# Performance work log

Measured on AMD Instinct MI355X. Metric: run time of the kernel, lower is better.

The kernel has to match this reference:

```python
import jax, jax.numpy as jnp
import numpy as np

NUM_HEADS = 16
NUM_KV_HEADS = 4
HEAD_DIM = 64
HIDDEN = 1024
B, S = 2, 2048


def setup_inputs() -> dict:
    key = jax.random.key(0)
    ks = jax.random.split(key, 9)
    sc = 0.02
    return {
        "x": jax.random.normal(ks[0], (B, S, HIDDEN), dtype=jnp.float32),
        "Wq": jax.random.normal(ks[1], (HIDDEN, NUM_HEADS * HEAD_DIM), dtype=jnp.float32) * sc,
        "bq": jnp.zeros((NUM_HEADS * HEAD_DIM,), dtype=jnp.float32),
        "Wk": jax.random.normal(ks[2], (HIDDEN, NUM_KV_HEADS * HEAD_DIM), dtype=jnp.float32) * sc,
        "bk": jnp.zeros((NUM_KV_HEADS * HEAD_DIM,), dtype=jnp.float32),
        "Wv": jax.random.normal(ks[3], (HIDDEN, NUM_KV_HEADS * HEAD_DIM), dtype=jnp.float32) * sc,
        "bv": jnp.zeros((NUM_KV_HEADS * HEAD_DIM,), dtype=jnp.float32),
        "Wo": jax.random.normal(ks[4], (NUM_HEADS * HEAD_DIM, HIDDEN), dtype=jnp.float32) * sc,
        "bo": jnp.zeros((HIDDEN,), dtype=jnp.float32),
    }


def reference(x, Wq, bq, Wk, bk, Wv, bv, Wo, bo):
    bs, seq, _ = x.shape
    groups = NUM_HEADS // NUM_KV_HEADS
    # projections -> [B, H, S, D]
    q = (x @ Wq + bq).reshape(bs, seq, NUM_HEADS, HEAD_DIM).transpose(0, 2, 1, 3)
    k = (x @ Wk + bk).reshape(bs, seq, NUM_KV_HEADS, HEAD_DIM).transpose(0, 2, 1, 3)
    v = (x @ Wv + bv).reshape(bs, seq, NUM_KV_HEADS, HEAD_DIM).transpose(0, 2, 1, 3)
    # repeat_interleave KV heads to match query heads (GQA expansion)
    k = jnp.repeat(k, groups, axis=1)
    v = jnp.repeat(v, groups, axis=1)
    # NOTE: source applies NO 1/sqrt(d) scaling and no mask/ALiBi
    scores = jnp.einsum("bhqd,bhkd->bhqk", q, k)
    attn = jax.nn.softmax(scores.astype(jnp.float32), axis=-1).astype(q.dtype)
    out = jnp.einsum("bhqk,bhkd->bhqd", attn, v)
    out = out.transpose(0, 2, 1, 3).reshape(bs, seq, NUM_HEADS * HEAD_DIM)
    return out @ Wo + bo
```

## Files before the change

kernel.cpp:

```cpp
#include <hip/hip_runtime.h>

#define NHEADS 16
#define NKV    4
#define HDIM   64
#define HIDDEN 1024
#define BATCH  2
#define SEQ    2048
#define MROWS  (BATCH * SEQ)
#define LOG2E  1.44269504088896340736f

typedef __bf16 bf16_t;
typedef bf16_t bf16x8 __attribute__((ext_vector_type(8)));
typedef float  f32x4  __attribute__((ext_vector_type(4)));

template<int N>  struct ic { static constexpr int  v = N; };
template<bool B> struct bc { static constexpr bool v = B; };

__device__ __forceinline__ float bf2f(unsigned short u) {
    return __uint_as_float(((unsigned int)u) << 16);
}
__device__ __forceinline__ unsigned short f2bf(float f) {
    unsigned int u = __float_as_uint(f);
    u += 0x7FFFu + ((u >> 16) & 1u);
    return (unsigned short)(u >> 16);
}

__device__ __forceinline__ void gld16(const unsigned short* g, unsigned short* l)
{
    __builtin_amdgcn_global_load_lds(
        (const __attribute__((address_space(1))) void*)g,
        (__attribute__((address_space(3))) void*)l,
        16, 0, 0);
}

__device__ __forceinline__ int swz(int row, int ch) {
    return (row * 8 + (ch ^ (row & 7))) * 8;
}

__device__ __forceinline__ bool sniff_is_f32(const unsigned short* __restrict__ x)
{
    const int e = (x[threadIdx.x & 63] >> 7) & 0xFF;
    const unsigned long long ok = __ballot(e >= 110 && e <= 140);
    return __popcll(ok) < 56;
}

__device__ __forceinline__ void load8cvt(const void* base, size_t elem, bool isf32, unsigned short out[8])
{
    if (!isf32) {
        *(uint4*)out = *(const uint4*)((const unsigned short*)base + elem);
    } else {
        const float* p = (const float*)base + elem;
        float4 v0 = *(const float4*)p;
        float4 v1 = *(const float4*)(p + 4);
        out[0] = f2bf(v0.x); out[1] = f2bf(v0.y); out[2] = f2bf(v0.z); out[3] = f2bf(v0.w);
        out[4] = f2bf(v1.x); out[5] = f2bf(v1.y); out[6] = f2bf(v1.z); out[7] = f2bf(v1.w);
    }
}
__device__ __forceinline__ float bias_at(const void* b, int i, bool isf32)
{
    return isf32 ? ((const float*)b)[i] : bf2f(((const unsigned short*)b)[i]);
}

__global__ __launch_bounds__(256)
void prep_kernel(const void* __restrict__ x,
                 const void* __restrict__ Wq, const void* __restrict__ Wk,
                 const void* __restrict__ Wv, const void* __restrict__ Wo,
                 unsigned short* __restrict__ xb,
                 unsigned short* __restrict__ Wqkvt,
                 unsigned short* __restrict__ Wot)
{
    const bool isf32 = sniff_is_f32((const unsigned short*)x);
    const int t = threadIdx.x;
    int bid = blockIdx.x;

    if (bid < 2048) {
        if (!isf32) return;
        const size_t c = (size_t)bid * 256 + t;
        unsigned short v[8];
        load8cvt(x, c * 8, true, v);
        *(uint4*)(&xb[c * 8]) = *(uint4*)v;
        return;
    }
    bid -= 2048;
    const void* src; unsigned short* dst; int N, rowoff;
    if (bid < 256)      {             src = Wq; dst = Wqkvt; N = 1024; rowoff = 0;    }
    else if (bid < 320) { bid -= 256; src = Wk; dst = Wqkvt; N = 256;  rowoff = 1024; }
    else if (bid < 384) { bid -= 320; src = Wv; dst = Wqkvt; N = 256;  rowoff = 1280; }
    else                { bid -= 384; src = Wo; dst = Wot;   N = 1024; rowoff = 0;    }
    const int ntx = N / 64;
    const int gn0 = (bid % ntx) * 64;
    const int gk0 = (bid / ntx) * 64;

    __shared__ unsigned short Ts[64][72];
#pragma unroll
    for (int half = 0; half < 2; ++half) {
        const int kl = (t >> 3) + half * 32;
        const int n8 = (t & 7) * 8;
        unsigned short v[8];
        load8cvt(src, (size_t)(gk0 + kl) * N + gn0 + n8, isf32, v);
        *(uint4*)(&Ts[kl][n8]) = *(uint4*)v;
    }
    __syncthreads();
#pragma unroll
    for (int half = 0; half < 2; ++half) {
        const int nl = (t >> 3) + half * 32;
        const int k8 = (t & 7) * 8;
        unsigned short v[8];
#pragma unroll
        for (int j = 0; j < 8; ++j) v[j] = Ts[k8 + j][nl];
        *(uint4*)(&dst[(size_t)(rowoff + gn0 + nl) * HIDDEN + gk0 + k8]) = *(uint4*)v;
    }
}

template<int AI, int BJ, int KK>
__device__ __forceinline__ void gemm_tile(const unsigned short* __restrict__ A,
                                          const unsigned short* __restrict__ Bt,
                                          int m0, int n0,
                                          unsigned short* As, unsigned short* Bs,
                                          f32x4 (&acc)[AI][BJ])
{
    const int tid  = threadIdx.x;
    const int lane = tid & 63;
    const int wave = tid >> 6;
    const int quad = lane >> 4;
    const int l15  = lane & 15;
    const int wr   = wave >> 1;
    const int wc   = wave & 1;

    const int srow = tid >> 3;
    const int gch  = ((tid & 7) ^ (srow & 7)) * 8;

    const unsigned short* ga[AI];
    const unsigned short* gb[BJ];
#pragma unroll
    for (int r = 0; r < AI; ++r) ga[r] = A  + (size_t)(m0 + r * 32 + srow) * KK + gch;
#pragma unroll
    for (int r = 0; r < BJ; ++r) gb[r] = Bt + (size_t)(n0 + r * 32 + srow) * KK + gch;

    unsigned short* const adst = As + wave * 512;
    unsigned short* const bdst = Bs + wave * 512;

    int aoffs[2][AI], boffs[2][BJ];
#pragma unroll
    for (int kk = 0; kk < 2; ++kk) {
#pragma unroll
        for (int i = 0; i < AI; ++i) aoffs[kk][i] = swz(wr * (AI * 16) + i * 16 + l15, kk * 4 + quad);
#pragma unroll
        for (int j = 0; j < BJ; ++j) boffs[kk][j] = swz(wc * (BJ * 16) + j * 16 + l15, kk * 4 + quad);
    }

    auto stage = [&](int buf) {
#pragma unroll
        for (int r = 0; r < AI; ++r) { gld16(ga[r], adst + buf * (AI * 2048) + r * 2048); ga[r] += 64; }
#pragma unroll
        for (int r = 0; r < BJ; ++r) { gld16(gb[r], bdst + buf * (BJ * 2048) + r * 2048); gb[r] += 64; }
    };

    constexpr int nk = KK / 64;
    stage(0);
#pragma unroll 2
    for (int k = 0; k < nk; ++k) {
        const int cur = k & 1;
        __syncthreads();
        if (k + 1 < nk) stage(cur ^ 1);

#pragma unroll
        for (int kk = 0; kk < 2; ++kk) {
            bf16x8 af[AI], bfv[BJ];
#pragma unroll
            for (int i = 0; i < AI; ++i) af[i]  = *(const bf16x8*)(&As[cur * (AI * 2048) + aoffs[kk][i]]);
#pragma unroll
            for (int j = 0; j < BJ; ++j) bfv[j] = *(const bf16x8*)(&Bs[cur * (BJ * 2048) + boffs[kk][j]]);
            __builtin_amdgcn_s_setprio(1);
#pragma unroll
            for (int i = 0; i < AI; ++i)
#pragma unroll
                for (int j = 0; j < BJ; ++j)
                    acc[i][j] = __builtin_amdgcn_mfma_f32_16x16x32_bf16(af[i], bfv[j], acc[i][j], 0, 0, 0);
            __builtin_amdgcn_s_setprio(0);
        }
    }
}

__global__ __launch_bounds__(256)
void gemm_qkv(const void* __restrict__ xraw,
              const unsigned short* __restrict__ xb,
              const unsigned short* __restrict__ Bt,
              const void* __restrict__ bq, const void* __restrict__ bk,
              const void* __restrict__ bv,
              unsigned short* __restrict__ Qh,
              unsigned short* __restrict__ Kh,
              unsigned short* __restrict__ Vt)
{
    __shared__ __align__(16) unsigned short As[2 * 128 * 64];
    __shared__ __align__(16) unsigned short Bs[2 * 96 * 64];
    const bool bias_f32 = sniff_is_f32((const unsigned short*)xraw);
    const unsigned short* A = bias_f32 ? xb : (const unsigned short*)xraw;
    const int lane = threadIdx.x & 63;
    const int wave = threadIdx.x >> 6;
    const int quad = lane >> 4, l15 = lane & 15;
    const int wr = wave >> 1, wc = wave & 1;
    const int m0 = blockIdx.y * 128, n0 = blockIdx.x * 96;

    f32x4 acc[4][3] = {};
    gemm_tile<4, 3, HIDDEN>(A, Bt, m0, n0, As, Bs, acc);

#pragma unroll
    for (int i = 0; i < 4; ++i) {
#pragma unroll
        for (int j = 0; j < 3; ++j) {
            const int nn  = n0 + wc * 48 + j * 16 + l15;
            const int mmb = m0 + wr * 64 + i * 16 + quad * 4;
            const int b = mmb >> 11, s0 = mmb & 2047;
            if (nn < 1024) {
                const float bias = bias_at(bq, nn, bias_f32);
                const int h = nn >> 6, d = nn & 63;
                const size_t idx0 = (((size_t)(b * NHEADS + h)) * SEQ + s0) * 64 + d;
#pragma unroll
                for (int r = 0; r < 4; ++r)
                    Qh[idx0 + (size_t)r * 64] = f2bf((acc[i][j][r] + bias) * LOG2E);
            } else if (nn < 1280) {
                const int nk = nn - 1024;
                const float bias = bias_at(bk, nk, bias_f32);
                const int h = nk >> 6, d = nk & 63;
                const size_t idx0 = (((size_t)(b * NKV + h)) * SEQ + s0) * 64 + d;
#pragma unroll
                for (int r = 0; r < 4; ++r)
                    Kh[idx0 + (size_t)r * 64] = f2bf(acc[i][j][r] + bias);
            } else {
                const int nv = nn - 1280;
                const float bias = bias_at(bv, nv, bias_f32);
                const int h = nv >> 6, d = nv & 63;
                const size_t idx = (((size_t)(b * NKV + h)) * 64 + d) * SEQ + s0;
                unsigned short vv[4];
#pragma unroll
                for (int r = 0; r < 4; ++r) vv[r] = f2bf(acc[i][j][r] + bias);
                *(uint2*)(&Vt[idx]) = *(uint2*)vv;
            }
        }
    }
}

__global__ __launch_bounds__(256)
void gemm_o(const void* __restrict__ xraw,
            const unsigned short* __restrict__ A,
            const unsigned short* __restrict__ Bt,
            const void* __restrict__ bo,
            float* __restrict__ out)
{
    __shared__ __align__(16) unsigned short As[2 * 128 * 64];
    __shared__ __align__(16) unsigned short Bs[2 * 64 * 64];
    const bool bias_f32 = sniff_is_f32((const unsigned short*)xraw);
    const int lane = threadIdx.x & 63;
    const int wave = threadIdx.x >> 6;
    const int quad = lane >> 4, l15 = lane & 15;
    const int wr = wave >> 1, wc = wave & 1;
    const int m0 = blockIdx.y * 128, n0 = blockIdx.x * 64;

    f32x4 acc[4][2] = {};
    gemm_tile<4, 2, HIDDEN>(A, Bt, m0, n0, As, Bs, acc);

#pragma unroll
    for (int i = 0; i < 4; ++i) {
#pragma unroll
        for (int j = 0; j < 2; ++j) {
            const int nn = n0 + wc * 32 + j * 16 + l15;
            const float bvv = bias_at(bo, nn, bias_f32);
#pragma unroll
            for (int r = 0; r < 4; ++r) {
                const int mm = m0 + wr * 64 + i * 16 + quad * 4 + r;
                out[(size_t)mm * HIDDEN + nn] = acc[i][j][r] + bvv;
            }
        }
    }
}

#define NT    (SEQ / 64)
#define KVOFF (64 * 64)

__global__ __launch_bounds__(256)
void attn_kernel(const unsigned short* __restrict__ Qh,
                 const unsigned short* __restrict__ Kh,
                 const unsigned short* __restrict__ Vt,
                 unsigned short* __restrict__ O)
{
    __shared__ __align__(16) unsigned short Kth[3 * KVOFF];
    __shared__ __align__(16) unsigned short VtT[3 * KVOFF];
    __shared__ __align__(16) unsigned short Pt[4 * 32 * 64];

    const int tid  = threadIdx.x;
    const int lane = tid & 63;
    const int wave = tid >> 6;
    const int quad = lane >> 4;
    const int l15  = lane & 15;

    const int qt = blockIdx.x;
    const int h  = blockIdx.y;
    const int b  = blockIdx.z;
    const int kv = h >> 2;

    const size_t qoff = ((size_t)(b * NHEADS + h)) * SEQ * HDIM;
    const size_t koff = ((size_t)(b * NKV + kv)) * SEQ * HDIM;
    const size_t voff = ((size_t)(b * NKV + kv)) * HDIM * SEQ;

    const int q0 = qt * 128 + wave * 32;

    bf16x8 qf0[2], qf1[2];
#pragma unroll
    for (int qs = 0; qs < 2; ++qs) {
        const size_t qrow = qoff + (size_t)(q0 + qs * 16 + l15) * HDIM;
        qf0[qs] = *(const bf16x8*)(&Qh[qrow + quad * 8]);
        qf1[qs] = *(const bf16x8*)(&Qh[qrow + 32 + quad * 8]);
    }

    bf16x8 onesv;
#pragma unroll
    for (int i = 0; i < 8; ++i) onesv[i] = (bf16_t)1.0f;

    f32x4 o0[4] = {}, o1[4] = {};
    f32x4 lacc0 = {}, lacc1 = {};

    int koff0[4], koff1[4], pwoff[2][4], proff[2], voffs[2][4];
#pragma unroll
    for (int j = 0; j < 4; ++j) {
        koff0[j] = swz(j * 16 + l15, quad);
        koff1[j] = swz(j * 16 + l15, quad ^ 4);
#pragma unroll
        for (int qs = 0; qs < 2; ++qs)
            pwoff[qs][j] = wave * 2048 + swz(qs * 16 + l15, j * 2 + (quad >> 1)) + (quad & 1) * 4;
    }
#pragma unroll
    for (int kk = 0; kk < 2; ++kk) {
        proff[kk] = wave * 2048 + swz(l15, kk * 4 + quad);
#pragma unroll
        for (int dt = 0; dt < 4; ++dt)
            voffs[kk][dt] = swz(dt * 16 + l15, kk * 4 + quad);
    }

    const unsigned short* kp = Kh + koff;
    const unsigned short* vp = Vt + voff;
    const int srow0 = tid >> 3;
    const int gch_s = ((tid & 7) ^ (srow0 & 7)) * 8;
    unsigned short* const kdst = Kth + wave * 512;
    unsigned short* const vdst = VtT + wave * 512;

#define ATTN_STAGE(B)                                                               \
    do {                                                                            \
        gld16(kp + (size_t)srow0 * HDIM + gch_s,        kdst + (B) * KVOFF);        \
        gld16(kp + (size_t)(srow0 + 32) * HDIM + gch_s, kdst + (B) * KVOFF + 2048); \
        gld16(vp + (size_t)srow0 * SEQ + gch_s,         vdst + (B) * KVOFF);        \
        gld16(vp + (size_t)(srow0 + 32) * SEQ + gch_s,  vdst + (B) * KVOFF + 2048); \
        kp += 64 * HDIM; vp += 64;                                                  \
    } while (0)

    ATTN_STAGE(0);
    ATTN_STAGE(1);

    auto step = [&](auto B_, auto STG_, auto LAST_) {
        constexpr int B = decltype(B_)::v;
        if constexpr (decltype(LAST_)::v) asm volatile("s_waitcnt vmcnt(0)" ::: "memory");
        else                              asm volatile("s_waitcnt vmcnt(4)" ::: "memory");
        __builtin_amdgcn_sched_barrier(0);
        __builtin_amdgcn_s_barrier();
        __builtin_amdgcn_sched_barrier(0);
        if constexpr (decltype(STG_)::v) ATTN_STAGE((B + 2) % 3);

#pragma unroll
        for (int j = 0; j < 4; ++j) {
            const bf16x8 kh0 = *(const bf16x8*)(&Kth[B * KVOFF + koff0[j]]);
            const bf16x8 kh1 = *(const bf16x8*)(&Kth[B * KVOFF + koff1[j]]);
#pragma unroll
            for (int qs = 0; qs < 2; ++qs) {
                f32x4 z = {};
                __builtin_amdgcn_s_setprio(1);
                z = __builtin_amdgcn_mfma_f32_16x16x32_bf16(kh0, qs ? qf0[1] : qf0[0], z, 0, 0, 0);
                const f32x4 sc = __builtin_amdgcn_mfma_f32_16x16x32_bf16(kh1, qs ? qf1[1] : qf1[0], z, 0, 0, 0);
                __builtin_amdgcn_s_setprio(0);
                const float p0 = __builtin_amdgcn_exp2f(sc[0]);
                const float p1 = __builtin_amdgcn_exp2f(sc[1]);
                const float p2 = __builtin_amdgcn_exp2f(sc[2]);
                const float p3 = __builtin_amdgcn_exp2f(sc[3]);
                uint2 w;
                w.x = __builtin_amdgcn_perm(__float_as_uint(p1), __float_as_uint(p0), 0x07060302u);
                w.y = __builtin_amdgcn_perm(__float_as_uint(p3), __float_as_uint(p2), 0x07060302u);
                *(uint2*)(&Pt[pwoff[qs][j]]) = w;
            }
        }

#pragma unroll
        for (int kk = 0; kk < 2; ++kk) {
            const bf16x8 pf0 = *(const bf16x8*)(&Pt[proff[kk]]);
            const bf16x8 pf1 = *(const bf16x8*)(&Pt[proff[kk] + 1024]);
            __builtin_amdgcn_s_setprio(1);
            lacc0 = __builtin_amdgcn_mfma_f32_16x16x32_bf16(onesv, pf0, lacc0, 0, 0, 0);
            lacc1 = __builtin_amdgcn_mfma_f32_16x16x32_bf16(onesv, pf1, lacc1, 0, 0, 0);
#pragma unroll
            for (int dt = 0; dt < 4; ++dt) {
                const bf16x8 vf = *(const bf16x8*)(&VtT[B * KVOFF + voffs[kk][dt]]);
                o0[dt] = __builtin_amdgcn_mfma_f32_16x16x32_bf16(vf, pf0, o0[dt], 0, 0, 0);
                o1[dt] = __builtin_amdgcn_mfma_f32_16x16x32_bf16(vf, pf1, o1[dt], 0, 0, 0);
            }
            __builtin_amdgcn_s_setprio(0);
        }
    };

#pragma unroll 1
    for (int t0 = 0; t0 < 30; t0 += 3) {
        step(ic<0>{}, bc<true>{}, bc<false>{});
        step(ic<1>{}, bc<true>{}, bc<false>{});
        step(ic<2>{}, bc<true>{}, bc<false>{});
    }
    step(ic<0>{}, bc<false>{}, bc<false>{});
    step(ic<1>{}, bc<false>{}, bc<true>{});
#undef ATTN_STAGE

#pragma unroll
    for (int qs = 0; qs < 2; ++qs) {
        const float inv = 1.0f / (qs ? lacc1[0] : lacc0[0]);
        const size_t rowbase = ((size_t)b * SEQ + (q0 + qs * 16 + l15)) * (NHEADS * HDIM) + h * HDIM;
#pragma unroll
        for (int dt = 0; dt < 4; ++dt) {
            const f32x4 ov = qs ? o1[dt] : o0[dt];
            unsigned short v4[4];
#pragma unroll
            for (int r = 0; r < 4; ++r) v4[r] = f2bf(ov[r] * inv);
            *(uint2*)(&O[rowbase + dt * 16 + quad * 4]) = *(uint2*)v4;
        }
    }
}

extern "C" void kernel_launch(void* const* d_in, const int* in_sizes, int n_in,
                              void* d_out, int out_size, void* d_ws, size_t ws_size,
                              hipStream_t stream)
{
    const void* x  = d_in[0];
    const void* Wq = d_in[1];
    const void* bq = d_in[2];
    const void* Wk = d_in[3];
    const void* bk = d_in[4];
    const void* Wv = d_in[5];
    const void* bv = d_in[6];
    const void* Wo = d_in[7];
    const void* bo = d_in[8];
    float* out = (float*)d_out;

    unsigned short* p = (unsigned short*)d_ws;
    unsigned short* xb    = p; p += (size_t)MROWS * HIDDEN;
    unsigned short* Wqkvt = p; p += (size_t)1536 * HIDDEN;
    unsigned short* Wot   = p; p += (size_t)HIDDEN * HIDDEN;
    unsigned short* Qh = p;  p += (size_t)MROWS * 1024;
    unsigned short* Kh = p;  p += (size_t)2 * NKV * SEQ * HDIM;
    unsigned short* Vt = p;  p += (size_t)2 * NKV * SEQ * HDIM;
    unsigned short* A2 = p;  p += (size_t)MROWS * 1024;

    dim3 blk(256);
    prep_kernel<<<dim3(2688), blk, 0, stream>>>(x, Wq, Wk, Wv, Wo, xb, Wqkvt, Wot);
    gemm_qkv<<<dim3(1536 / 96, MROWS / 128), blk, 0, stream>>>(
        x, xb, Wqkvt, bq, bk, bv, Qh, Kh, Vt);
    attn_kernel<<<dim3(SEQ / 128, NHEADS, BATCH), blk, 0, stream>>>(Qh, Kh, Vt, A2);
    gemm_o<<<dim3(1024 / 64, MROWS / 128), blk, 0, stream>>>(x, A2, Wot, bo, out);
}
```

Before: 177.8 us.

## Load K fragments directly into registers in attention; shrink QKV GEMM N-tile

The attention kernel stops staging K tiles through LDS and instead loads each wave's K MFMA fragments straight from global memory into a double-buffered register set, while V keeps its three-stage LDS pipeline. The wait counts and the step schedule are rewritten to interleave the two buffer rotations. This drops LDS traffic and shared memory use for K, at the cost of redundant global reads of K by all four waves and more VGPRs. Separately, the QKV GEMM tile width goes from 96 to 64 columns, giving more blocks.

```diff
diff --git a/kernel.cpp b/kernel.cpp
--- a/kernel.cpp
+++ b/kernel.cpp
@@ -193,23 +193,23 @@
               unsigned short* __restrict__ Vt)
 {
     __shared__ __align__(16) unsigned short As[2 * 128 * 64];
-    __shared__ __align__(16) unsigned short Bs[2 * 96 * 64];
+    __shared__ __align__(16) unsigned short Bs[2 * 64 * 64];
     const bool bias_f32 = sniff_is_f32((const unsigned short*)xraw);
     const unsigned short* A = bias_f32 ? xb : (const unsigned short*)xraw;
     const int lane = threadIdx.x & 63;
     const int wave = threadIdx.x >> 6;
     const int quad = lane >> 4, l15 = lane & 15;
     const int wr = wave >> 1, wc = wave & 1;
-    const int m0 = blockIdx.y * 128, n0 = blockIdx.x * 96;
-
-    f32x4 acc[4][3] = {};
-    gemm_tile<4, 3, HIDDEN>(A, Bt, m0, n0, As, Bs, acc);
+    const int m0 = blockIdx.y * 128, n0 = blockIdx.x * 64;
+
+    f32x4 acc[4][2] = {};
+    gemm_tile<4, 2, HIDDEN>(A, Bt, m0, n0, As, Bs, acc);
 
 #pragma unroll
     for (int i = 0; i < 4; ++i) {
 #pragma unroll
-        for (int j = 0; j < 3; ++j) {
-            const int nn  = n0 + wc * 48 + j * 16 + l15;
+        for (int j = 0; j < 2; ++j) {
+            const int nn  = n0 + wc * 32 + j * 16 + l15;
             const int mmb = m0 + wr * 64 + i * 16 + quad * 4;
             const int b = mmb >> 11, s0 = mmb & 2047;
             if (nn < 1024) {
@@ -284,7 +284,6 @@
                  const unsigned short* __restrict__ Vt,
                  unsigned short* __restrict__ O)
 {
-    __shared__ __align__(16) unsigned short Kth[3 * KVOFF];
     __shared__ __align__(16) unsigned short VtT[3 * KVOFF];
     __shared__ __align__(16) unsigned short Pt[4 * 32 * 64];
 
@@ -320,15 +319,12 @@
     f32x4 o0[4] = {}, o1[4] = {};
     f32x4 lacc0 = {}, lacc1 = {};
 
-    int koff0[4], koff1[4], pwoff[2][4], proff[2], voffs[2][4];
-#pragma unroll
-    for (int j = 0; j < 4; ++j) {
-        koff0[j] = swz(j * 16 + l15, quad);
-        koff1[j] = swz(j * 16 + l15, quad ^ 4);
+    int pwoff[2][4], proff[2], voffs[2][4];
+#pragma unroll
+    for (int j = 0; j < 4; ++j)
 #pragma unroll
         for (int qs = 0; qs < 2; ++qs)
             pwoff[qs][j] = wave * 2048 + swz(qs * 16 + l15, j * 2 + (quad >> 1)) + (quad & 1) * 4;
-    }
 #pragma unroll
     for (int kk = 0; kk < 2; ++kk) {
         proff[kk] = wave * 2048 + swz(l15, kk * 4 + quad);
@@ -337,44 +333,55 @@
             voffs[kk][dt] = swz(dt * 16 + l15, kk * 4 + quad);
     }
 
-    const unsigned short* kp = Kh + koff;
-    const unsigned short* vp = Vt + voff;
+    const unsigned short* kfp = Kh + koff + (size_t)l15 * HDIM + quad * 8;
+    const unsigned short* vp  = Vt + voff;
     const int srow0 = tid >> 3;
     const int gch_s = ((tid & 7) ^ (srow0 & 7)) * 8;
-    unsigned short* const kdst = Kth + wave * 512;
     unsigned short* const vdst = VtT + wave * 512;
 
-#define ATTN_STAGE(B)                                                               \
-    do {                                                                            \
-        gld16(kp + (size_t)srow0 * HDIM + gch_s,        kdst + (B) * KVOFF);        \
-        gld16(kp + (size_t)(srow0 + 32) * HDIM + gch_s, kdst + (B) * KVOFF + 2048); \
-        gld16(vp + (size_t)srow0 * SEQ + gch_s,         vdst + (B) * KVOFF);        \
-        gld16(vp + (size_t)(srow0 + 32) * SEQ + gch_s,  vdst + (B) * KVOFF + 2048); \
-        kp += 64 * HDIM; vp += 64;                                                  \
+    bf16x8 kr0[2][4], kr1[2][4];
+
+#define KLOAD(KB)                                                                \
+    do {                                                                         \
+        _Pragma("unroll")                                                        \
+        for (int j = 0; j < 4; ++j) {                                            \
+            kr0[KB][j] = *(const bf16x8*)(kfp + j * (16 * HDIM));                \
+            kr1[KB][j] = *(const bf16x8*)(kfp + j * (16 * HDIM) + 32);           \
+        }                                                                        \
+        kfp += 64 * HDIM;                                                        \
     } while (0)
 
-    ATTN_STAGE(0);
-    ATTN_STAGE(1);
-
-    auto step = [&](auto B_, auto STG_, auto LAST_) {
-        constexpr int B = decltype(B_)::v;
+#define VSTAGE(B)                                                                \
+    do {                                                                         \
+        gld16(vp + (size_t)srow0 * SEQ + gch_s,        vdst + (B) * KVOFF);      \
+        gld16(vp + (size_t)(srow0 + 32) * SEQ + gch_s, vdst + (B) * KVOFF + 2048); \
+        vp += 64;                                                                \
+    } while (0)
+
+    VSTAGE(0);
+    KLOAD(0);
+    VSTAGE(1);
+
+    auto step = [&](auto VB_, auto KB_, auto SV_, auto SK_, auto LAST_) {
+        constexpr int VB = decltype(VB_)::v;
+        constexpr int KB = decltype(KB_)::v;
         if constexpr (decltype(LAST_)::v) asm volatile("s_waitcnt vmcnt(0)" ::: "memory");
-        else                              asm volatile("s_waitcnt vmcnt(4)" ::: "memory");
+        else                              asm volatile("s_waitcnt vmcnt(10)" ::: "memory");
         __builtin_amdgcn_sched_barrier(0);
         __builtin_amdgcn_s_barrier();
         __builtin_amdgcn_sched_barrier(0);
-        if constexpr (decltype(STG_)::v) ATTN_STAGE((B + 2) % 3);
+        if constexpr (decltype(SK_)::v) KLOAD(KB ^ 1);
+        if constexpr (decltype(SV_)::v) VSTAGE((VB + 2) % 3);
+        __builtin_amdgcn_sched_barrier(0);
 
 #pragma unroll
         for (int j = 0; j < 4; ++j) {
-            const bf16x8 kh0 = *(const bf16x8*)(&Kth[B * KVOFF + koff0[j]]);
-            const bf16x8 kh1 = *(const bf16x8*)(&Kth[B * KVOFF + koff1[j]]);
 #pragma unroll
             for (int qs = 0; qs < 2; ++qs) {
                 f32x4 z = {};
                 __builtin_amdgcn_s_setprio(1);
-                z = __builtin_amdgcn_mfma_f32_16x16x32_bf16(kh0, qs ? qf0[1] : qf0[0], z, 0, 0, 0);
-                const f32x4 sc = __builtin_amdgcn_mfma_f32_16x16x32_bf16(kh1, qs ? qf1[1] : qf1[0], z, 0, 0, 0);
+                z = __builtin_amdgcn_mfma_f32_16x16x32_bf16(kr0[KB][j], qs ? qf0[1] : qf0[0], z, 0, 0, 0);
+                const f32x4 sc = __builtin_amdgcn_mfma_f32_16x16x32_bf16(kr1[KB][j], qs ? qf1[1] : qf1[0], z, 0, 0, 0);
                 __builtin_amdgcn_s_setprio(0);
                 const float p0 = __builtin_amdgcn_exp2f(sc[0]);
                 const float p1 = __builtin_amdgcn_exp2f(sc[1]);
@@ -396,7 +403,7 @@
             lacc1 = __builtin_amdgcn_mfma_f32_16x16x32_bf16(onesv, pf1, lacc1, 0, 0, 0);
 #pragma unroll
             for (int dt = 0; dt < 4; ++dt) {
-                const bf16x8 vf = *(const bf16x8*)(&VtT[B * KVOFF + voffs[kk][dt]]);
+                const bf16x8 vf = *(const bf16x8*)(&VtT[VB * KVOFF + voffs[kk][dt]]);
                 o0[dt] = __builtin_amdgcn_mfma_f32_16x16x32_bf16(vf, pf0, o0[dt], 0, 0, 0);
                 o1[dt] = __builtin_amdgcn_mfma_f32_16x16x32_bf16(vf, pf1, o1[dt], 0, 0, 0);
             }
@@ -405,14 +412,18 @@
     };
 
 #pragma unroll 1
-    for (int t0 = 0; t0 < 30; t0 += 3) {
-        step(ic<0>{}, bc<true>{}, bc<false>{});
-        step(ic<1>{}, bc<true>{}, bc<false>{});
-        step(ic<2>{}, bc<true>{}, bc<false>{});
-    }
-    step(ic<0>{}, bc<false>{}, bc<false>{});
-    step(ic<1>{}, bc<false>{}, bc<true>{});
-#undef ATTN_STAGE
+    for (int t0 = 0; t0 < 30; t0 += 6) {
+        step(ic<0>{}, ic<0>{}, bc<true>{}, bc<true>{}, bc<false>{});
+        step(ic<1>{}, ic<1>{}, bc<true>{}, bc<true>{}, bc<false>{});
+        step(ic<2>{}, ic<0>{}, bc<true>{}, bc<true>{}, bc<false>{});
+        step(ic<0>{}, ic<1>{}, bc<true>{}, bc<true>{}, bc<false>{});
+        step(ic<1>{}, ic<0>{}, bc<true>{}, bc<true>{}, bc<false>{});
+        step(ic<2>{}, ic<1>{}, bc<true>{}, bc<true>{}, bc<false>{});
+    }
+    step(ic<0>{}, ic<0>{}, bc<false>{}, bc<true>{},  bc<false>{});
+    step(ic<1>{}, ic<1>{}, bc<false>{}, bc<false>{}, bc<true>{});
+#undef KLOAD
+#undef VSTAGE
 
 #pragma unroll
     for (int qs = 0; qs < 2; ++qs) {
@@ -455,7 +466,7 @@
 
     dim3 blk(256);
     prep_kernel<<<dim3(2688), blk, 0, stream>>>(x, Wq, Wk, Wv, Wo, xb, Wqkvt, Wot);
-    gemm_qkv<<<dim3(1536 / 96, MROWS / 128), blk, 0, stream>>>(
+    gemm_qkv<<<dim3(1536 / 64, MROWS / 128), blk, 0, stream>>>(
         x, xb, Wqkvt, bq, bk, bv, Qh, Kh, Vt);
     attn_kernel<<<dim3(SEQ / 128, NHEADS, BATCH), blk, 0, stream>>>(Qh, Kh, Vt, A2);
     gemm_o<<<dim3(1024 / 64, MROWS / 128), blk, 0, stream>>>(x, A2, Wot, bo, out);
```

Result: slower. 196.7 us (+10.6%).
